# Performance work log

Measured on AMD Instinct MI355X. Metric: run time of the kernel, lower is better.

Reference implementation:

```python
import jax, jax.numpy as jnp
import numpy as np
import math

NUM_HEADS = 16
THETA = 10000.0

def setup_inputs() -> dict:
    key = jax.random.key(0)
    ks = jax.random.split(key, 5)
    B, S, D = 2, 2048, 1024
    sigma = math.sqrt(2.0 / (D + D))
    return {
        "x": jax.random.normal(ks[0], (B, S, D), dtype=jnp.float32),
        "token_positions": jnp.arange(B * S, dtype=jnp.int64 if jax.config.jax_enable_x64 else jnp.int32).reshape(B, S),
        "Wq": jax.random.normal(ks[1], (D, D), dtype=jnp.float32) * sigma,
        "Wk": jax.random.normal(ks[2], (D, D), dtype=jnp.float32) * sigma,
        "Wv": jax.random.normal(ks[3], (D, D), dtype=jnp.float32) * sigma,
        "Wo": jax.random.normal(ks[4], (D, D), dtype=jnp.float32) * sigma,
    }

def _rotate_half_interleaved(t):
    # pairs (x0,x1) -> (-x1, x0), interleaved layout as in the torch module
    *lead, d = t.shape
    t2 = t.reshape(*lead, d // 2, 2)
    r = jnp.stack([-t2[..., 1], t2[..., 0]], axis=-1)
    return r.reshape(*lead, d)

def reference(x, token_positions, Wq, Wk, Wv, Wo):
    B, S, D = x.shape
    H = NUM_HEADS
    hd = D // H

    # QKV projections (Linear stores weight as [out, in])
    q = (x @ Wq.T).reshape(B, S, H, hd).transpose(0, 2, 1, 3)  # [B,H,S,hd]
    k = (x @ Wk.T).reshape(B, S, H, hd).transpose(0, 2, 1, 3)
    v = (x @ Wv.T).reshape(B, S, H, hd).transpose(0, 2, 1, 3)

    # RoPE: inv_freq over even indices of head_dim
    inv_freq = 1.0 / (THETA ** (jnp.arange(0, hd, 2, dtype=jnp.float32) / hd))  # [hd/2]
    ang = token_positions.astype(jnp.float32)[..., None] * inv_freq  # [B,S,hd/2]
    cos = jnp.repeat(jnp.cos(ang), 2, axis=-1)[:, None]  # [B,1,S,hd]
    sin = jnp.repeat(jnp.sin(ang), 2, axis=-1)[:, None]
    q = q * cos + _rotate_half_interleaved(q) * sin
    k = k * cos + _rotate_half_interleaved(k) * sin

    # causal attention (full scores materialized, matching the torch module)
    scores = jnp.einsum('bhqd,bhkd->bhqk', q, k) / jnp.sqrt(jnp.float32(hd))
    causal = jnp.tril(jnp.ones((S, S), dtype=bool))
    scores = jnp.where(causal, scores, -jnp.inf)
    probs = jax.nn.softmax(scores, axis=-1)
    att = jnp.einsum('bhqk,bhkd->bhqd', probs, v)  # [B,H,S,hd]

    out = att.transpose(0, 2, 1, 3).reshape(B, S, D) @ Wo.T
    return out
```

## Files before the change

kernel.cpp:

```cpp
#include <hip/hip_runtime.h>
#include <hip/hip_bf16.h>

typedef __bf16 bf16;
typedef __bf16 bf16x4 __attribute__((ext_vector_type(4)));
typedef __bf16 bf16x8 __attribute__((ext_vector_type(8)));
typedef float f32x4 __attribute__((ext_vector_type(4)));
typedef float f32x16 __attribute__((ext_vector_type(16)));
typedef unsigned int u32x4 __attribute__((ext_vector_type(4)));

#define NH 16
#define HD 64
#define SEQ 2048
#define DM 1024
#define MTOT 4096

__device__ __forceinline__ void gload_lds16(const void* g, void* l) {
  __builtin_amdgcn_global_load_lds(
      (const __attribute__((address_space(1))) void*)g,
      (__attribute__((address_space(3))) void*)l, 16, 0, 0);
}

__global__ void cvt_kernel(const float* __restrict__ in, bf16* __restrict__ out, int n4) {
  int i = blockIdx.x * blockDim.x + threadIdx.x;
  if (i >= n4) return;
  float4 v = reinterpret_cast<const float4*>(in)[i];
  bf16x4 o;
  o[0] = (bf16)v.x; o[1] = (bf16)v.y; o[2] = (bf16)v.z; o[3] = (bf16)v.w;
  *reinterpret_cast<bf16x4*>(out + (size_t)i * 4) = o;
}

__global__ void cvt4_kernel(const float* __restrict__ w0, const float* __restrict__ w1,
                            const float* __restrict__ w2, const float* __restrict__ w3,
                            bf16* __restrict__ out) {
  int i = blockIdx.x * blockDim.x + threadIdx.x;
  int seg = i >> 18;
  int j = i & 262143;
  const float* src = seg == 0 ? w0 : seg == 1 ? w1 : seg == 2 ? w2 : w3;
  float4 v = reinterpret_cast<const float4*>(src)[j];
  bf16x4 o;
  o[0] = (bf16)v.x; o[1] = (bf16)v.y; o[2] = (bf16)v.z; o[3] = (bf16)v.w;
  *reinterpret_cast<bf16x4*>(out + ((size_t)seg << 20) + (size_t)j * 4) = o;
}

__global__ void rope_tab_kernel(const int* __restrict__ pos, float2* __restrict__ tab) {
  int i = blockIdx.x * blockDim.x + threadIdx.x;
  if (i >= MTOT * 32) return;
  int m = i >> 5, i2 = i & 31;
  float pf = (float)pos[m];
  float inv = 1.0f / powf(10000.0f, (float)(2 * i2) * (1.0f / 64.0f));
  float a = pf * inv;
  tab[i] = make_float2(cosf(a), sinf(a));
}

__global__ __launch_bounds__(512) void gemm_qkv(
    const bf16* __restrict__ A, const bf16* __restrict__ wAll,
    bf16* __restrict__ outq, bf16* __restrict__ outk, bf16* __restrict__ outv,
    const float2* __restrict__ tab)
{
  __shared__ bf16 As[2][256 * 32];
  __shared__ bf16 Bs[2][256 * 32];
  const int t = threadIdx.x;
  const int w = t >> 6;
  const int wm = w >> 2, wn = w & 3;
  const int lane = t & 63;
  const int lr = lane & 15;
  const int lg = lane >> 4;
  const int m0 = blockIdx.y * 256;
  const int proj = blockIdx.x >> 2;
  const int n0l = (blockIdx.x & 3) * 256;
  const char* Ab = (const char*)A;
  const char* Bb = (const char*)(wAll + ((size_t)proj << 20) + (size_t)n0l * DM);

  f32x4 acc[8][4] = {};

#define STAGE_QKV(KT, SLOT)                                                       \
  {                                                                               \
    _Pragma("unroll")                                                             \
    for (int p = 0; p < 2; ++p) {                                                 \
      int o = (p * 512 + t) * 16;                                                 \
      int r = o >> 6, cb = o & 63;                                                \
      gload_lds16(Ab + (size_t)(m0 + r) * 2048 + (KT) * 64 + cb,                  \
                  (char*)As[SLOT] + o);                                           \
    }                                                                             \
    _Pragma("unroll")                                                             \
    for (int p = 0; p < 2; ++p) {                                                 \
      int o = (p * 512 + t) * 16;                                                 \
      int r = o >> 6, cb = o & 63;                                                \
      gload_lds16(Bb + (size_t)r * 2048 + (KT) * 64 + cb, (char*)Bs[SLOT] + o);   \
    }                                                                             \
  }

  STAGE_QKV(0, 0);
  for (int kt = 0; kt < 32; ++kt) {
    if (kt + 1 < 32) {
      STAGE_QKV(kt + 1, (kt + 1) & 1);
      asm volatile("s_waitcnt vmcnt(4)" ::: "memory");
    } else {
      asm volatile("s_waitcnt vmcnt(0)" ::: "memory");
    }
    __builtin_amdgcn_sched_barrier(0);
    __builtin_amdgcn_s_barrier();

    const bf16* Abuf = As[kt & 1];
    const bf16* Bbuf = Bs[kt & 1];
    bf16x8 af[8], bfr[4];
#pragma unroll
    for (int i = 0; i < 8; ++i)
      af[i] = *reinterpret_cast<const bf16x8*>(Abuf + (wm * 128 + i * 16 + lr) * 32 + lg * 8);
#pragma unroll
    for (int j = 0; j < 4; ++j)
      bfr[j] = *reinterpret_cast<const bf16x8*>(Bbuf + (wn * 64 + j * 16 + lr) * 32 + lg * 8);
    __builtin_amdgcn_s_setprio(1);
#pragma unroll
    for (int i = 0; i < 8; ++i)
#pragma unroll
      for (int j = 0; j < 4; ++j)
        acc[i][j] = __builtin_amdgcn_mfma_f32_16x16x32_bf16(af[i], bfr[j], acc[i][j], 0, 0, 0);
    __builtin_amdgcn_s_setprio(0);
    __builtin_amdgcn_s_barrier();
  }

  if (proj < 2) {
    bf16* outb = proj ? outk : outq;
#pragma unroll
    for (int j = 0; j < 4; ++j) {
      int nl = n0l + wn * 64 + j * 16 + lr;
      int h = nl >> 6, d = nl & 63;
      int i2 = d >> 1;
      bool odd = d & 1;
#pragma unroll
      for (int i = 0; i < 8; ++i) {
#pragma unroll
        for (int rr = 0; rr < 4; ++rr) {
          int m = m0 + wm * 128 + i * 16 + lg * 4 + rr;
          float v = acc[i][j][rr];
          float o = __shfl_xor(v, 1);
          float2 cs = tab[(m << 5) + i2];
          float res = odd ? (v * cs.x + o * cs.y) : (v * cs.x - o * cs.y);
          if (proj == 0) res *= 0.125f * 1.44269504f;
          outb[((size_t)((m >> 11) * NH + h) * SEQ + (m & 2047)) * HD + d] = (bf16)res;
        }
      }
    }
  } else {
#pragma unroll
    for (int j = 0; j < 4; ++j) {
      int nl = n0l + wn * 64 + j * 16 + lr;
      int h = nl >> 6, d = nl & 63;
#pragma unroll
      for (int i = 0; i < 8; ++i) {
#pragma unroll
        for (int rr = 0; rr < 4; ++rr) {
          int m = m0 + wm * 128 + i * 16 + lg * 4 + rr;
          outv[((size_t)((m >> 11) * NH + h) * HD + d) * SEQ + (m & 2047)] = (bf16)acc[i][j][rr];
        }
      }
    }
  }
#undef STAGE_QKV
}

__global__ __launch_bounds__(256) void gemm_out(
    const bf16* __restrict__ A, const bf16* __restrict__ Bw, float* __restrict__ outf)
{
  __shared__ bf16 As[2][128 * 32];
  __shared__ bf16 Bs[2][128 * 32];
  const int t = threadIdx.x;
  const int w = t >> 6;
  const int lane = t & 63;
  const int lr = lane & 15;
  const int lg = lane >> 4;
  const int m0 = blockIdx.y * 128;
  const int n0 = blockIdx.x * 128;
  const int wr = w >> 1, wc = w & 1;
  const char* Bb = (const char*)Bw;

  f32x4 acc[4][4] = {};

#define STAGE_OUT(KT, SLOT)                                                            \
  {                                                                                    \
    _Pragma("unroll")                                                                  \
    for (int p = 0; p < 2; ++p) {                                                      \
      int o = (p * 256 + t) * 16;                                                      \
      int r = o >> 6, cb = o & 63;                                                     \
      int m = m0 + r;                                                                  \
      const char* ga = (const char*)A +                                                \
          ((((size_t)(m >> 11) * NH + ((KT) >> 1)) * SEQ + (m & 2047)) * HD +          \
           ((KT) & 1) * 32) * 2 + cb;                                                  \
      gload_lds16(ga, (char*)As[SLOT] + o);                                            \
    }                                                                                  \
    _Pragma("unroll")                                                                  \
    for (int p = 0; p < 2; ++p) {                                                      \
      int o = (p * 256 + t) * 16;                                                      \
      int r = o >> 6, cb = o & 63;                                                     \
      gload_lds16(Bb + (size_t)(n0 + r) * 2048 + (KT) * 64 + cb, (char*)Bs[SLOT] + o); \
    }                                                                                  \
  }

  STAGE_OUT(0, 0);
  for (int kt = 0; kt < 32; ++kt) {
    if (kt + 1 < 32) {
      STAGE_OUT(kt + 1, (kt + 1) & 1);
      asm volatile("s_waitcnt vmcnt(4)" ::: "memory");
    } else {
      asm volatile("s_waitcnt vmcnt(0)" ::: "memory");
    }
    __builtin_amdgcn_sched_barrier(0);
    __builtin_amdgcn_s_barrier();

    const bf16* Abuf = As[kt & 1];
    const bf16* Bbuf = Bs[kt & 1];
    bf16x8 af[4], bfr[4];
#pragma unroll
    for (int f = 0; f < 4; ++f) {
      af[f]  = *reinterpret_cast<const bf16x8*>(Abuf + (wr * 64 + f * 16 + lr) * 32 + lg * 8);
      bfr[f] = *reinterpret_cast<const bf16x8*>(Bbuf + (wc * 64 + f * 16 + lr) * 32 + lg * 8);
    }
    __builtin_amdgcn_s_setprio(1);
#pragma unroll
    for (int i = 0; i < 4; ++i)
#pragma unroll
      for (int j = 0; j < 4; ++j)
        acc[i][j] = __builtin_amdgcn_mfma_f32_16x16x32_bf16(af[i], bfr[j], acc[i][j], 0, 0, 0);
    __builtin_amdgcn_s_setprio(0);
    __builtin_amdgcn_s_barrier();
  }

#pragma unroll
  for (int j = 0; j < 4; ++j) {
    int n = n0 + wc * 64 + j * 16 + lr;
#pragma unroll
    for (int i = 0; i < 4; ++i) {
#pragma unroll
      for (int rr = 0; rr < 4; ++rr) {
        int m = m0 + wr * 64 + i * 16 + lg * 4 + rr;
        outf[(size_t)m * DM + n] = acc[i][j][rr];
      }
    }
  }
#undef STAGE_OUT
}

__device__ __forceinline__ void stage512(const char* gRow0, size_t rowStrideB, int colByte0,
                                         char* lds, int t) {
  int o = t * 16;
  int r = o >> 7;
  int cb = o & 127;
  int cbs = cb ^ ((r & 7) << 4);
  gload_lds16(gRow0 + (size_t)r * rowStrideB + colByte0 + cbs, lds + o);
}

__device__ __forceinline__ bf16x8 frag64(const char* tile, int row, int colByte) {
  int b = row * 128 + (colByte ^ ((row & 7) << 4));
  return *reinterpret_cast<const bf16x8*>(tile + b);
}

__device__ __forceinline__ unsigned packw(float a, float b) {
  unsigned short la = __builtin_bit_cast(unsigned short, (bf16)a);
  unsigned short lb = __builtin_bit_cast(unsigned short, (bf16)b);
  return (unsigned)la | ((unsigned)lb << 16);
}

__device__ __forceinline__ void tile_step(const char* Kt, const char* Vt,
                                          const bf16x8* qf,
                                          f32x16& acc0, f32x16& acc1,
                                          float& mrow, float& lrow,
                                          int l31, int h, bool domask, int qloc) {
  f32x16 s0 = {}, s1 = {};
  __builtin_amdgcn_s_setprio(1);
#pragma unroll
  for (int s = 0; s < 4; ++s) {
    bf16x8 kf0 = frag64(Kt, l31, s * 32 + h * 16);
    bf16x8 kf1 = frag64(Kt, 32 + l31, s * 32 + h * 16);
    s0 = __builtin_amdgcn_mfma_f32_32x32x16_bf16(kf0, qf[s], s0, 0, 0, 0);
    s1 = __builtin_amdgcn_mfma_f32_32x32x16_bf16(kf1, qf[s], s1, 0, 0, 0);
  }
  __builtin_amdgcn_s_setprio(0);
  if (domask) {
#pragma unroll
    for (int reg = 0; reg < 16; ++reg) {
      int ro = (reg & 3) + 8 * (reg >> 2) + 4 * h;
      if (ro > qloc) s0[reg] = -1e30f;
      if (ro + 32 > qloc) s1[reg] = -1e30f;
    }
  }
  float tm[16];
#pragma unroll
  for (int i = 0; i < 16; ++i) tm[i] = fmaxf(s0[i], s1[i]);
#pragma unroll
  for (int off = 8; off >= 1; off >>= 1)
#pragma unroll
    for (int i = 0; i < off; ++i) tm[i] = fmaxf(tm[i], tm[i + off]);
  float rmax = fmaxf(tm[0], __shfl_xor(tm[0], 32));
  bool need = __any(rmax > mrow + 11.5f);
  if (need) {
    float mnew = fmaxf(mrow, rmax);
    float osc = exp2f(mrow - mnew);
#pragma unroll
    for (int reg = 0; reg < 16; ++reg) {
      int rs = (reg & 3) + 8 * (reg >> 2) + 4 * h;
      float o = __shfl(osc, rs);
      acc0[reg] *= o;
      acc1[reg] *= o;
    }
    lrow *= osc;
    mrow = mnew;
  }
#pragma unroll
  for (int i = 0; i < 16; ++i) {
    s0[i] = exp2f(s0[i] - mrow);
    s1[i] = exp2f(s1[i] - mrow);
  }
  float ts[16];
#pragma unroll
  for (int i = 0; i < 16; ++i) ts[i] = s0[i] + s1[i];
#pragma unroll
  for (int off = 8; off >= 1; off >>= 1)
#pragma unroll
    for (int i = 0; i < off; ++i) ts[i] += ts[i + off];
  lrow += ts[0] + __shfl_xor(ts[0], 32);

  unsigned W0[4][2], W1[4][2], X0[4][2], X1[4][2];
#pragma unroll
  for (int sp = 0; sp < 4; ++sp)
#pragma unroll
    for (int u = 0; u < 2; ++u) {
      W0[sp][u] = packw(s0[sp * 4 + 2 * u], s0[sp * 4 + 2 * u + 1]);
      W1[sp][u] = packw(s1[sp * 4 + 2 * u], s1[sp * 4 + 2 * u + 1]);
    }
#pragma unroll
  for (int sp = 0; sp < 4; ++sp)
#pragma unroll
    for (int u = 0; u < 2; ++u) {
      X0[sp][u] = (unsigned)__shfl_xor((int)W0[sp][u], 32);
      X1[sp][u] = (unsigned)__shfl_xor((int)W1[sp][u], 32);
    }
  __builtin_amdgcn_s_setprio(1);
#pragma unroll
  for (int ks = 0; ks < 4; ++ks) {
    const unsigned (*W)[2] = (ks < 2) ? W0 : W1;
    const unsigned (*X)[2] = (ks < 2) ? X0 : X1;
    const int c = ks & 1;
    unsigned m0 = h ? X[2 * c + 1][0] : W[2 * c][0];
    unsigned m1 = h ? X[2 * c + 1][1] : W[2 * c][1];
    unsigned m2 = h ? W[2 * c + 1][0] : X[2 * c][0];
    unsigned m3 = h ? W[2 * c + 1][1] : X[2 * c][1];
    u32x4 pw = {m0, m1, m2, m3};
    bf16x8 pf = __builtin_bit_cast(bf16x8, pw);
    bf16x8 vf0 = frag64(Vt, l31, ks * 32 + h * 16);
    bf16x8 vf1 = frag64(Vt, 32 + l31, ks * 32 + h * 16);
    acc0 = __builtin_amdgcn_mfma_f32_32x32x16_bf16(pf, vf0, acc0, 0, 0, 0);
    acc1 = __builtin_amdgcn_mfma_f32_32x32x16_bf16(pf, vf1, acc1, 0, 0, 0);
  }
  __builtin_amdgcn_s_setprio(0);
}

__global__ __launch_bounds__(512, 4) void attn_kernel(
    const bf16* __restrict__ q, const bf16* __restrict__ k,
    const bf16* __restrict__ vt, bf16* __restrict__ att)
{
  __shared__ __align__(16) char pool[65536];
  const int t = threadIdx.x;
  const int w = t >> 6;
  const int wsub = w & 3;
  const int par = w >> 2;
  const int lane = t & 63;
  const int l31 = lane & 31;
  const int h = lane >> 5;

  const int idx = blockIdx.x;
  const int half = idx >> 8;
  const int sub = idx & 255;
  const int bh = sub & 31;
  const int j = half ? (sub >> 5) : (15 - (sub >> 5));

  const int strip = 2 * j + (wsub >> 1);
  const int myN = strip + 1;
  const int npair = j + 1;
  const int q0w = j * 128 + wsub * 32;
  const int qloc = (wsub & 1) * 32 + l31;

  const bf16* qb = q + (size_t)bh * SEQ * HD;
  const char* kbB = (const char*)(k + (size_t)bh * SEQ * HD);
  const char* vbB = (const char*)(vt + (size_t)bh * HD * SEQ);

  bf16x8 qf[4];
#pragma unroll
  for (int s = 0; s < 4; ++s)
    qf[s] = *reinterpret_cast<const bf16x8*>(qb + (size_t)(q0w + l31) * HD + s * 16 + h * 8);

  f32x16 acc0 = {}, acc1 = {};
  float mrow = -1e30f, lrow = 0.f;

  stage512(kbB, 128, 0, pool + 0 * 8192, t);
  stage512(vbB, 4096, 0, pool + 32768 + 0 * 8192, t);
  stage512(kbB + 8192, 128, 0, pool + 1 * 8192, t);
  stage512(vbB, 4096, 128, pool + 32768 + 1 * 8192, t);
  if (npair > 1) {
    stage512(kbB + 2 * 8192, 128, 0, pool + 2 * 8192, t);
    stage512(vbB, 4096, 2 * 128, pool + 32768 + 2 * 8192, t);
    stage512(kbB + 3 * 8192, 128, 0, pool + 3 * 8192, t);
    stage512(vbB, 4096, 3 * 128, pool + 32768 + 3 * 8192, t);
  }

  for (int u = 0; u < npair; ++u) {
    if (u < npair - 1) {
      asm volatile("s_waitcnt vmcnt(4)" ::: "memory");
    } else {
      asm volatile("s_waitcnt vmcnt(0)" ::: "memory");
    }
    __builtin_amdgcn_sched_barrier(0);
    __builtin_amdgcn_s_barrier();

    const int tt = 2 * u + par;
    if (tt < myN)
      tile_step(pool + (tt & 3) * 8192, pool + 32768 + (tt & 3) * 8192, qf,
                acc0, acc1, mrow, lrow, l31, h, tt == strip, qloc);

    __builtin_amdgcn_s_barrier();
    __builtin_amdgcn_sched_barrier(0);
    if (u + 2 < npair) {
      int nt = 2 * u + 4;
      stage512(kbB + (size_t)nt * 8192, 128, 0, pool + (nt & 3) * 8192, t);
      stage512(vbB, 4096, nt * 128, pool + 32768 + (nt & 3) * 8192, t);
      stage512(kbB + (size_t)(nt + 1) * 8192, 128, 0, pool + ((nt + 1) & 3) * 8192, t);
      stage512(vbB, 4096, (nt + 1) * 128, pool + 32768 + ((nt + 1) & 3) * 8192, t);
    }
  }

  float* mb = (float*)pool;
  float* reg = mb + wsub * (34 * 64);
  if (par == 1) {
#pragma unroll
    for (int i = 0; i < 16; ++i) reg[i * 64 + lane] = acc0[i];
#pragma unroll
    for (int i = 0; i < 16; ++i) reg[(16 + i) * 64 + lane] = acc1[i];
    reg[32 * 64 + lane] = mrow;
    reg[33 * 64 + lane] = lrow;
  }
  __syncthreads();
  if (par == 0) {
    float mB = reg[32 * 64 + lane];
    float lB = reg[33 * 64 + lane];
    float mM = fmaxf(mrow, mB);
    float alpha = exp2f(mrow - mM);
    float beta  = exp2f(mB - mM);
    float linv = 1.0f / (alpha * lrow + beta * lB);
#pragma unroll
    for (int rg = 0; rg < 16; ++rg) {
      int rs = (rg & 3) + 8 * (rg >> 2) + 4 * h;
      float a  = __shfl(alpha, rs);
      float b  = __shfl(beta, rs);
      float li = __shfl(linv, rs);
      float o0 = (a * acc0[rg] + b * reg[rg * 64 + lane]) * li;
      float o1 = (a * acc1[rg] + b * reg[(16 + rg) * 64 + lane]) * li;
      size_t base = ((size_t)bh * SEQ + q0w + rs) * HD;
      att[base + l31]      = (bf16)o0;
      att[base + 32 + l31] = (bf16)o1;
    }
  }
}

extern "C" void kernel_launch(void* const* d_in, const int* in_sizes, int n_in,
                              void* d_out, int out_size, void* d_ws, size_t ws_size,
                              hipStream_t stream) {
  const float* x  = (const float*)d_in[0];
  const int* pos  = (const int*)d_in[1];
  const float* Wq = (const float*)d_in[2];
  const float* Wk = (const float*)d_in[3];
  const float* Wv = (const float*)d_in[4];
  const float* Wo = (const float*)d_in[5];
  float* out = (float*)d_out;

  char* p = (char*)d_ws;
  bf16* xb   = (bf16*)p; p += (size_t)MTOT * DM * 2;
  bf16* wqb  = (bf16*)p; p += (size_t)DM * DM * 2;
  bf16* wkb  = (bf16*)p; p += (size_t)DM * DM * 2;
  bf16* wvb  = (bf16*)p; p += (size_t)DM * DM * 2;
  bf16* wob  = (bf16*)p; p += (size_t)DM * DM * 2;
  bf16* qb   = (bf16*)p; p += (size_t)MTOT * DM * 2;
  bf16* kb   = (bf16*)p; p += (size_t)MTOT * DM * 2;
  bf16* vtb  = (bf16*)p; p += (size_t)MTOT * DM * 2;
  bf16* attb = (bf16*)p; p += (size_t)MTOT * DM * 2;
  float2* tab = (float2*)p; p += (size_t)MTOT * 32 * sizeof(float2);
  (void)wkb; (void)wvb;

  cvt_kernel<<<(MTOT * DM / 4 + 255) / 256, 256, 0, stream>>>(x, xb, MTOT * DM / 4);
  cvt4_kernel<<<(4 * 262144 + 255) / 256, 256, 0, stream>>>(Wq, Wk, Wv, Wo, wqb);
  rope_tab_kernel<<<(MTOT * 32 + 255) / 256, 256, 0, stream>>>(pos, tab);

  gemm_qkv<<<dim3(12, MTOT / 256), 512, 0, stream>>>(xb, wqb, qb, kb, vtb, tab);

  attn_kernel<<<512, 512, 0, stream>>>(qb, kb, vtb, attb);

  gemm_out<<<dim3(DM / 128, MTOT / 128), 256, 0, stream>>>(attb, wob, out);
}
```

Baseline: 140.5 us.

## Deepen QKV GEMM pipeline with swizzled LDS and finer-grained phases

Rewrites the QKV projection GEMM main loop to use K-tiles of 64 split into two 32-wide halves, with a deeper multi-stage LDS buffer (128 KB) and XOR-swizzled LDS layout to avoid bank conflicts. Each iteration is split into eight phases that interleave half-tile global->LDS staging with MFMA work on half of the M fragments, so loads are issued continuously. It also sets launch_bounds occupancy hint of 2, though the larger LDS footprint may limit occupancy and the extra barriers add sync overhead.

```diff
diff --git a/kernel.cpp b/kernel.cpp
--- a/kernel.cpp
+++ b/kernel.cpp
@@ -52,13 +52,12 @@
   tab[i] = make_float2(cosf(a), sinf(a));
 }
 
-__global__ __launch_bounds__(512) void gemm_qkv(
+__global__ __launch_bounds__(512, 2) void gemm_qkv(
     const bf16* __restrict__ A, const bf16* __restrict__ wAll,
     bf16* __restrict__ outq, bf16* __restrict__ outk, bf16* __restrict__ outv,
     const float2* __restrict__ tab)
 {
-  __shared__ bf16 As[2][256 * 32];
-  __shared__ bf16 Bs[2][256 * 32];
+  __shared__ bf16 ABlds[2][2][2][8192];
   const int t = threadIdx.x;
   const int w = t >> 6;
   const int wm = w >> 2, wn = w & 3;
@@ -68,57 +67,98 @@
   const int m0 = blockIdx.y * 256;
   const int proj = blockIdx.x >> 2;
   const int n0l = (blockIdx.x & 3) * 256;
-  const char* Ab = (const char*)A;
-  const char* Bb = (const char*)(wAll + ((size_t)proj << 20) + (size_t)n0l * DM);
+  const char* Asrc = (const char*)A + (size_t)m0 * 2048;
+  const char* Bsrc = (const char*)(wAll + ((size_t)proj << 20) + (size_t)n0l * DM);
 
   f32x4 acc[8][4] = {};
-
-#define STAGE_QKV(KT, SLOT)                                                       \
-  {                                                                               \
-    _Pragma("unroll")                                                             \
-    for (int p = 0; p < 2; ++p) {                                                 \
-      int o = (p * 512 + t) * 16;                                                 \
-      int r = o >> 6, cb = o & 63;                                                \
-      gload_lds16(Ab + (size_t)(m0 + r) * 2048 + (KT) * 64 + cb,                  \
-                  (char*)As[SLOT] + o);                                           \
-    }                                                                             \
-    _Pragma("unroll")                                                             \
-    for (int p = 0; p < 2; ++p) {                                                 \
-      int o = (p * 512 + t) * 16;                                                 \
-      int r = o >> 6, cb = o & 63;                                                \
-      gload_lds16(Bb + (size_t)r * 2048 + (KT) * 64 + cb, (char*)Bs[SLOT] + o);   \
-    }                                                                             \
-  }
-
-  STAGE_QKV(0, 0);
-  for (int kt = 0; kt < 32; ++kt) {
-    if (kt + 1 < 32) {
-      STAGE_QKV(kt + 1, (kt + 1) & 1);
-      asm volatile("s_waitcnt vmcnt(4)" ::: "memory");
-    } else {
-      asm volatile("s_waitcnt vmcnt(0)" ::: "memory");
-    }
-    __builtin_amdgcn_sched_barrier(0);
-    __builtin_amdgcn_s_barrier();
-
-    const bf16* Abuf = As[kt & 1];
-    const bf16* Bbuf = Bs[kt & 1];
-    bf16x8 af[8], bfr[4];
-#pragma unroll
-    for (int i = 0; i < 8; ++i)
-      af[i] = *reinterpret_cast<const bf16x8*>(Abuf + (wm * 128 + i * 16 + lr) * 32 + lg * 8);
-#pragma unroll
-    for (int j = 0; j < 4; ++j)
-      bfr[j] = *reinterpret_cast<const bf16x8*>(Bbuf + (wn * 64 + j * 16 + lr) * 32 + lg * 8);
-    __builtin_amdgcn_s_setprio(1);
-#pragma unroll
-    for (int i = 0; i < 8; ++i)
-#pragma unroll
-      for (int j = 0; j < 4; ++j)
-        acc[i][j] = __builtin_amdgcn_mfma_f32_16x16x32_bf16(af[i], bfr[j], acc[i][j], 0, 0, 0);
-    __builtin_amdgcn_s_setprio(0);
-    __builtin_amdgcn_s_barrier();
-  }
+  bf16x8 bfr[4];
+
+#define REG(AB_, PAR_, KK_) ((char*)ABlds + (((AB_)*4 + (PAR_)*2 + (KK_)) * 16384))
+
+#define STAGE_HALF(AB_, T_, KK_)                                                   \
+  {                                                                                \
+    const char* gb_ = (AB_) ? Bsrc : Asrc;                                         \
+    char* lb_ = REG(AB_, (T_) & 1, KK_);                                           \
+    _Pragma("unroll")                                                              \
+    for (int p_ = 0; p_ < 2; ++p_) {                                               \
+      int o_ = (p_ * 512 + t) * 16;                                                \
+      int r_ = o_ >> 6, c_ = o_ & 63;                                              \
+      int cs_ = c_ ^ (((r_ >> 1) & 3) << 4);                                       \
+      gload_lds16(gb_ + (size_t)r_ * 2048 + (T_) * 128 + (KK_) * 64 + cs_,         \
+                  lb_ + o_);                                                       \
+    }                                                                              \
+  }
+
+#define RDFRAG(DST, REGP, ROW)                                                     \
+  {                                                                                \
+    int row_ = (ROW);                                                              \
+    int cb_ = (lg * 16) ^ (((row_ >> 1) & 3) << 4);                                \
+    DST = *reinterpret_cast<const bf16x8*>((REGP) + row_ * 64 + cb_);              \
+  }
+
+#define PHASE(PAR, KK, MH, DOSTAGE, S_AB, S_T, S_KK, VM)                           \
+  {                                                                                \
+    bf16x8 af_[4];                                                                 \
+    const char* areg_ = REG(0, PAR, KK);                                           \
+    _Pragma("unroll")                                                              \
+    for (int f_ = 0; f_ < 4; ++f_)                                                 \
+      RDFRAG(af_[f_], areg_, wm * 128 + (MH) * 64 + f_ * 16 + lr);                 \
+    if ((MH) == 0) {                                                               \
+      const char* breg_ = REG(1, PAR, KK);                                         \
+      _Pragma("unroll")                                                            \
+      for (int j_ = 0; j_ < 4; ++j_)                                               \
+        RDFRAG(bfr[j_], breg_, wn * 64 + j_ * 16 + lr);                            \
+    }                                                                              \
+    if (DOSTAGE) STAGE_HALF(S_AB, S_T, S_KK);                                      \
+    if ((VM) == 8) asm volatile("s_waitcnt vmcnt(8)" ::: "memory");                \
+    if ((VM) == 4) asm volatile("s_waitcnt vmcnt(4)" ::: "memory");                \
+    if ((VM) == 0) asm volatile("s_waitcnt vmcnt(0)" ::: "memory");                \
+    __builtin_amdgcn_sched_barrier(0);                                             \
+    __builtin_amdgcn_s_barrier();                                                  \
+    asm volatile("s_waitcnt lgkmcnt(0)" ::: "memory");                             \
+    __builtin_amdgcn_sched_barrier(0);                                             \
+    __builtin_amdgcn_s_setprio(1);                                                 \
+    _Pragma("unroll")                                                              \
+    for (int f_ = 0; f_ < 4; ++f_)                                                 \
+      _Pragma("unroll")                                                            \
+      for (int j_ = 0; j_ < 4; ++j_)                                               \
+        acc[(MH) * 4 + f_][j_] = __builtin_amdgcn_mfma_f32_16x16x32_bf16(          \
+            af_[f_], bfr[j_], acc[(MH) * 4 + f_][j_], 0, 0, 0);                    \
+    __builtin_amdgcn_s_setprio(0);                                                 \
+    __builtin_amdgcn_s_barrier();                                                  \
+  }
+
+  STAGE_HALF(0, 0, 0); STAGE_HALF(1, 0, 0);
+  STAGE_HALF(0, 0, 1); STAGE_HALF(1, 0, 1);
+  STAGE_HALF(0, 1, 0); STAGE_HALF(1, 1, 0);
+  asm volatile("s_waitcnt vmcnt(4)" ::: "memory");
+  __builtin_amdgcn_sched_barrier(0);
+  __builtin_amdgcn_s_barrier();
+
+  for (int i = 0; i < 7; ++i) {
+    const int t1 = 2 * i + 1, t2 = 2 * i + 2, t3 = 2 * i + 3;
+    PHASE(0, 0, 0, 1, 0, t1, 1, -1);
+    PHASE(0, 0, 1, 1, 1, t1, 1,  8);
+    PHASE(0, 1, 0, 1, 0, t2, 0, -1);
+    PHASE(0, 1, 1, 1, 1, t2, 0,  8);
+    PHASE(1, 0, 0, 1, 0, t2, 1, -1);
+    PHASE(1, 0, 1, 1, 1, t2, 1,  8);
+    PHASE(1, 1, 0, 1, 0, t3, 0, -1);
+    PHASE(1, 1, 1, 1, 1, t3, 0,  8);
+  }
+  PHASE(0, 0, 0, 1, 0, 15, 1, -1);
+  PHASE(0, 0, 1, 1, 1, 15, 1,  8);
+  PHASE(0, 1, 0, 0, 0, 0, 0, -1);
+  PHASE(0, 1, 1, 0, 0, 0, 0,  4);
+  PHASE(1, 0, 0, 0, 0, 0, 0, -1);
+  PHASE(1, 0, 1, 0, 0, 0, 0,  0);
+  PHASE(1, 1, 0, 0, 0, 0, 0, -1);
+  PHASE(1, 1, 1, 0, 0, 0, 0, -1);
+
+#undef PHASE
+#undef RDFRAG
+#undef STAGE_HALF
+#undef REG
 
   if (proj < 2) {
     bf16* outb = proj ? outk : outq;
@@ -157,7 +197,6 @@
       }
     }
   }
-#undef STAGE_QKV
 }
 
 __global__ __launch_bounds__(256) void gemm_out(
```

Measured after the change: 126.6 us. -9.9%, faster.
